# Performance work log

Measured on AMD Instinct MI355X. Metric: run time of the kernel, lower is better.

## Reference

```python
import jax, jax.numpy as jnp
import numpy as np

N_NODES = 100000
N_EDGES = 1600000
D_FEAT = 32


def setup_inputs() -> dict:
    key = jax.random.key(0)
    k1, k2, k3 = jax.random.split(key, 3)
    return {
        "x_real": jax.random.normal(k1, (N_NODES, D_FEAT), dtype=jnp.float32),
        "x_imag": jax.random.normal(k2, (N_NODES, D_FEAT), dtype=jnp.float32),
        "edge_index": jax.random.randint(k3, (2, N_EDGES), 0, N_NODES, dtype=jnp.int64),
        "evolution_time": jnp.asarray(0.5, dtype=jnp.float32),
        "diffusion_strength": jnp.asarray(1.0, dtype=jnp.float32),
    }


def reference(x_real, x_imag, edge_index, evolution_time, diffusion_strength):
    eps = 1e-8
    num_nodes = x_real.shape[0]
    x = x_real + 1j * x_imag  # [N, D] complex64

    # add self loops
    loops = jnp.arange(num_nodes, dtype=edge_index.dtype)
    row = jnp.concatenate([edge_index[0], loops])  # [E+N]
    col = jnp.concatenate([edge_index[1], loops])  # [E+N]

    # symmetric degree normalization: deg computed over col (as in source)
    deg = jnp.zeros((num_nodes,), jnp.float32).at[col].add(1.0)
    deg_inv_sqrt = jnp.where(deg > 0, deg ** -0.5, 0.0)
    norm = (deg_inv_sqrt[row] * deg_inv_sqrt[col])[:, None]  # [E+N, 1]

    def propagate(h):
        # gather by col, scale, scatter-add by row
        msgs = h[col] * norm.astype(h.dtype)
        return jnp.zeros_like(h).at[row].add(msgs)

    first_order = propagate(x)
    coeff1 = 1j * (evolution_time * diffusion_strength)
    evolved = x + coeff1 * first_order

    # evolution_order >= 2 (second-order Taylor term)
    second_order = propagate(first_order)
    evolved = evolved + (coeff1 * coeff1) * 0.5 * second_order

    # per-node |psi|^2 weights, normalized to sum to num_nodes
    w = (evolved * jnp.conj(evolved)).real.sum(axis=-1, keepdims=True)  # [N,1]
    s = w.sum()
    w = jnp.where(s > eps, w / s * num_nodes, jnp.ones_like(w))
    return w, evolved
```

## Files before the change

### kernel.cpp

```cpp
#include <hip/hip_runtime.h>
#include <cstdint>
#include <cstddef>


#define TPB 256
#define BSL 64
#define CRANGE 16384
#define SRANGE 8192

typedef _Float16 h2 __attribute__((ext_vector_type(2)));

#if defined(__has_builtin)
#if __has_builtin(__builtin_amdgcn_fdot2)
#define HAS_FDOT2 1
#endif
#endif

__device__ __forceinline__ h2 u2h(uint32_t u) {
    union { uint32_t u; h2 h; } x; x.u = u; return x.h;
}
__device__ __forceinline__ uint32_t h2u(h2 h) {
    union { uint32_t u; h2 h; } x; x.h = h; return x.u;
}
__device__ __forceinline__ uint32_t packh(float re, float im) {
    h2 h; h.x = (_Float16)re; h.y = (_Float16)im; return h2u(h);
}
__device__ __forceinline__ void acc2(uint32_t p, float& aR, float& aI) {
#ifdef HAS_FDOT2
    h2 v = u2h(p);
    h2 LO; LO.x = (_Float16)1.0f; LO.y = (_Float16)0.0f;
    h2 HI; HI.x = (_Float16)0.0f; HI.y = (_Float16)1.0f;
    aR = __builtin_amdgcn_fdot2(v, LO, aR, false);
    aI = __builtin_amdgcn_fdot2(v, HI, aI, false);
#else
    h2 v = u2h(p);
    aR += (float)v.x;
    aI += (float)v.y;
#endif
}
__device__ __forceinline__ void acc4(uint4 p, float (&aR)[4], float (&aI)[4]) {
    acc2(p.x, aR[0], aI[0]);
    acc2(p.y, aR[1], aI[1]);
    acc2(p.z, aR[2], aI[2]);
    acc2(p.w, aR[3], aI[3]);
}

__device__ __forceinline__ int slice_len(int E) {
    return (((E + BSL - 1) / BSL) + 3) & ~3;
}

__global__ void k_cnt2(const int* __restrict__ col, const int* __restrict__ row,
                       int E, int Nw, uint32_t* __restrict__ parts_col,
                       uint32_t* __restrict__ parts_row) {
    __shared__ uint32_t sh[CRANGE / 2];
    int which = blockIdx.x & 1;
    int rb = blockIdx.x >> 1;
    int r = rb / BSL, b = rb % BSL;
    const int* keys = which ? row : col;
    uint32_t*  parts = which ? parts_row : parts_col;
    int rbase = r * CRANGE;
    for (int i = threadIdx.x; i < CRANGE / 2; i += TPB) sh[i] = 0;
    __syncthreads();
    int SL = slice_len(E);
    int s0 = b * SL, s1 = min(E, s0 + SL);
    int n = s1 - s0;
    if (n > 0) {
        const int4* k4 = (const int4*)(keys + s0);
        int n4 = n >> 2;
        for (int j = threadIdx.x; j < n4; j += TPB) {
            int4 v = k4[j];
            int k;
            k = v.x - rbase; if ((unsigned)k < CRANGE) atomicAdd(&sh[k >> 1], 1u << ((k & 1) * 16));
            k = v.y - rbase; if ((unsigned)k < CRANGE) atomicAdd(&sh[k >> 1], 1u << ((k & 1) * 16));
            k = v.z - rbase; if ((unsigned)k < CRANGE) atomicAdd(&sh[k >> 1], 1u << ((k & 1) * 16));
            k = v.w - rbase; if ((unsigned)k < CRANGE) atomicAdd(&sh[k >> 1], 1u << ((k & 1) * 16));
        }
        for (int e = s0 + (n4 << 2) + threadIdx.x; e < s1; e += TPB) {
            int k = keys[e] - rbase;
            if ((unsigned)k < CRANGE) atomicAdd(&sh[k >> 1], 1u << ((k & 1) * 16));
        }
    }
    __syncthreads();
    int wbase = rbase >> 1;
    for (int i = threadIdx.x; i < CRANGE / 2; i += TPB) {
        int w = wbase + i;
        if (w < Nw) parts[(size_t)b * Nw + w] = sh[i];
    }
}

__global__ void k_discol(const uint32_t* __restrict__ parts, int Nw, int N,
                         float* __restrict__ dis) {
    int w = blockIdx.x * blockDim.x + threadIdx.x;
    if (w >= Nw) return;
    uint32_t lo = 0, hi = 0;
    for (int b = 0; b < BSL; ++b) {
        uint32_t v = parts[(size_t)b * Nw + w];
        lo += v & 0xFFFFu; hi += v >> 16;
    }
    int n = 2 * w;
    if (n < N)     dis[n]     = rsqrtf((float)lo + 1.0f);
    if (n + 1 < N) dis[n + 1] = rsqrtf((float)hi + 1.0f);
}

__global__ void k_redrow(const uint32_t* __restrict__ parts, int Nw, int N,
                         unsigned char* __restrict__ sliceoff,
                         int* __restrict__ rowcnt) {
    int w = blockIdx.x * blockDim.x + threadIdx.x;
    if (w >= Nw) return;
    uint32_t lo = 0, hi = 0;
    int n = 2 * w;
    for (int b = 0; b < BSL; ++b) {
        uint32_t v = parts[(size_t)b * Nw + w];
        if (n < N)     sliceoff[(size_t)b * N + n]     = (unsigned char)lo;
        if (n + 1 < N) sliceoff[(size_t)b * N + n + 1] = (unsigned char)hi;
        lo += v & 0xFFFFu; hi += v >> 16;
    }
    if (n < N)     rowcnt[n]     = (int)lo;
    if (n + 1 < N) rowcnt[n + 1] = (int)hi;
}

__global__ void k_scan1(const int* __restrict__ in, int* __restrict__ out,
                        int* __restrict__ partials, int N) {
    __shared__ int sh[256];
    int t = threadIdx.x;
    int base = blockIdx.x * 1024 + t * 4;
    int v0 = (base + 0 < N) ? in[base + 0] : 0;
    int v1 = (base + 1 < N) ? in[base + 1] : 0;
    int v2 = (base + 2 < N) ? in[base + 2] : 0;
    int v3 = (base + 3 < N) ? in[base + 3] : 0;
    int s = v0 + v1 + v2 + v3;
    sh[t] = s;
    __syncthreads();
    for (int off = 1; off < 256; off <<= 1) {
        int add = (t >= off) ? sh[t - off] : 0;
        __syncthreads();
        sh[t] += add;
        __syncthreads();
    }
    int excl = sh[t] - s;
    if (base + 0 < N) out[base + 0] = excl;
    excl += v0;
    if (base + 1 < N) out[base + 1] = excl;
    excl += v1;
    if (base + 2 < N) out[base + 2] = excl;
    excl += v2;
    if (base + 3 < N) out[base + 3] = excl;
    if (t == 255) partials[blockIdx.x] = sh[255];
}

__global__ void k_scan2(int* __restrict__ partials, int nb) {
    if (threadIdx.x == 0 && blockIdx.x == 0) {
        int acc = 0;
        for (int i = 0; i < nb; ++i) { int v = partials[i]; partials[i] = acc; acc += v; }
    }
}

__global__ void k_scan3(int* __restrict__ out, const int* __restrict__ partials,
                        int N, int E) {
    int i = blockIdx.x * blockDim.x + threadIdx.x;
    if (i < N) out[i] += partials[i >> 10];
    if (i == 0) out[N] = E;
}

__global__ void k_scatter2(const int* __restrict__ row, const int* __restrict__ col,
                           int E, int N, const int* __restrict__ rowptr,
                           const unsigned char* __restrict__ sliceoff,
                           int* __restrict__ ecol) {
    __shared__ int cur[SRANGE];
    int r = blockIdx.x / BSL, b = blockIdx.x % BSL;
    int rbase = r * SRANGE;
    for (int i = threadIdx.x; i < SRANGE; i += TPB) {
        int n = rbase + i;
        cur[i] = (n < N) ? rowptr[n] + (int)sliceoff[(size_t)b * N + n] : 0;
    }
    __syncthreads();
    int SL = slice_len(E);
    int s0 = b * SL, s1 = min(E, s0 + SL);
    int n = s1 - s0;
    if (n <= 0) return;
    const int4* r4 = (const int4*)(row + s0);
    const int4* c4 = (const int4*)(col + s0);
    int n4 = n >> 2;
    for (int j = threadIdx.x; j < n4; j += TPB) {
        int4 rv = r4[j];
        int4 cv = c4[j];
        int rr;
        rr = rv.x - rbase; if ((unsigned)rr < SRANGE) ecol[atomicAdd(&cur[rr], 1)] = cv.x;
        rr = rv.y - rbase; if ((unsigned)rr < SRANGE) ecol[atomicAdd(&cur[rr], 1)] = cv.y;
        rr = rv.z - rbase; if ((unsigned)rr < SRANGE) ecol[atomicAdd(&cur[rr], 1)] = cv.z;
        rr = rv.w - rbase; if ((unsigned)rr < SRANGE) ecol[atomicAdd(&cur[rr], 1)] = cv.w;
    }
    for (int e = s0 + (n4 << 2) + threadIdx.x; e < s1; e += TPB) {
        int rr = row[e] - rbase;
        if ((unsigned)rr < SRANGE) ecol[atomicAdd(&cur[rr], 1)] = col[e];
    }
}

__global__ void k_pack(const float* __restrict__ xr, const float* __restrict__ xi,
                       const float* __restrict__ dis, uint32_t* __restrict__ xds,
                       int N) {
    int i = blockIdx.x * blockDim.x + threadIdx.x;
    if (i < N * 32) {
        int n = i >> 5, k = i & 31, s = k >> 3, dd = k & 7;
        float dg = dis[n];
        xds[((size_t)s * N + n) * 8 + dd] = packh(xr[i] * dg, xi[i] * dg);
    }
}

__device__ __forceinline__ void edge_accum4(const int* __restrict__ ecol,
                                            const uint4* __restrict__ hb4,
                                            int beg, int end, int epos, int half,
                                            float (&aR)[4], float (&aI)[4]) {
    int base = beg;
    for (; base + 16 <= end; base += 16) {
        int c0 = ecol[base + epos];
        int c1 = ecol[base + epos + 4];
        int c2 = ecol[base + epos + 8];
        int c3 = ecol[base + epos + 12];
        uint4 p0 = hb4[(size_t)c0 * 2 + half];
        uint4 p1 = hb4[(size_t)c1 * 2 + half];
        uint4 p2 = hb4[(size_t)c2 * 2 + half];
        uint4 p3 = hb4[(size_t)c3 * 2 + half];
        acc4(p0, aR, aI); acc4(p1, aR, aI);
        acc4(p2, aR, aI); acc4(p3, aR, aI);
    }
    if (base + 8 <= end) {
        int c0 = ecol[base + epos];
        int c1 = ecol[base + epos + 4];
        uint4 p0 = hb4[(size_t)c0 * 2 + half];
        uint4 p1 = hb4[(size_t)c1 * 2 + half];
        acc4(p0, aR, aI); acc4(p1, aR, aI);
        base += 8;
    }
    int rem = end - base;
    if (epos < rem) {
        int c = ecol[base + epos];
        uint4 p = hb4[(size_t)c * 2 + half];
        acc4(p, aR, aI);
    }
    if (epos + 4 < rem) {
        int c = ecol[base + epos + 4];
        uint4 p = hb4[(size_t)c * 2 + half];
        acc4(p, aR, aI);
    }
}

__device__ __forceinline__ void reduce8(float (&aR)[4], float (&aI)[4]) {
    #pragma unroll
    for (int d = 0; d < 4; ++d) {
        aR[d] += __shfl_xor(aR[d], 2, 8);
        aI[d] += __shfl_xor(aI[d], 2, 8);
        aR[d] += __shfl_xor(aR[d], 4, 8);
        aI[d] += __shfl_xor(aI[d], 4, 8);
    }
}

__global__ void k_p1(const int* __restrict__ rowptr, const int* __restrict__ ecol,
                     const float* __restrict__ dis, const uint32_t* __restrict__ xds,
                     uint32_t* __restrict__ fo2b, uint32_t* __restrict__ fods, int N) {
    int s   = blockIdx.x & 3;
    int nb  = blockIdx.x >> 2;
    int r   = nb * 32 + (threadIdx.x >> 3);
    int sub = threadIdx.x & 7;
    int half = sub & 1, epos = sub >> 1;
    if (r >= N) return;
    const uint4* hb4 = (const uint4*)(xds + (size_t)s * N * 8);
    int beg = rowptr[r], end = rowptr[r + 1];
    float dg = dis[r];
    float aR[4] = {0.f, 0.f, 0.f, 0.f}, aI[4] = {0.f, 0.f, 0.f, 0.f};
    edge_accum4(ecol, hb4, beg, end, epos, half, aR, aI);
    reduce8(aR, aI);
    acc4(hb4[(size_t)r * 2 + half], aR, aI);
    if (epos == 0) {
        float foR[4], foI[4];
        #pragma unroll
        for (int d = 0; d < 4; ++d) { foR[d] = dg * aR[d]; foI[d] = dg * aI[d]; }
        uint4 f, fd;
        f.x = packh(foR[0], foI[0]); f.y = packh(foR[1], foI[1]);
        f.z = packh(foR[2], foI[2]); f.w = packh(foR[3], foI[3]);
        fd.x = packh(foR[0] * dg, foI[0] * dg); fd.y = packh(foR[1] * dg, foI[1] * dg);
        fd.z = packh(foR[2] * dg, foI[2] * dg); fd.w = packh(foR[3] * dg, foI[3] * dg);
        ((uint4*)(fo2b + (size_t)s * N * 8))[(size_t)r * 2 + half] = f;
        ((uint4*)(fods + (size_t)s * N * 8))[(size_t)r * 2 + half] = fd;
    }
}

__global__ void k_p2(const int* __restrict__ rowptr, const int* __restrict__ ecol,
                     const float* __restrict__ dis, const uint32_t* __restrict__ fo2b,
                     const uint32_t* __restrict__ fods,
                     const float* __restrict__ tptr, const float* __restrict__ dptr,
                     uint32_t* __restrict__ delta, int N) {
    int s   = blockIdx.x & 3;
    int nb  = blockIdx.x >> 2;
    int r   = nb * 32 + (threadIdx.x >> 3);
    int sub = threadIdx.x & 7;
    int half = sub & 1, epos = sub >> 1;
    if (r >= N) return;
    const uint4* hb4 = (const uint4*)(fods + (size_t)s * N * 8);
    int beg = rowptr[r], end = rowptr[r + 1];
    float dg = dis[r];
    float aR[4] = {0.f, 0.f, 0.f, 0.f}, aI[4] = {0.f, 0.f, 0.f, 0.f};
    edge_accum4(ecol, hb4, beg, end, epos, half, aR, aI);
    reduce8(aR, aI);
    acc4(hb4[(size_t)r * 2 + half], aR, aI);
    if (epos == 0) {
        float c1  = tptr[0] * dptr[0];
        float c2h = 0.5f * c1 * c1;
        uint4 f = ((const uint4*)(fo2b + (size_t)s * N * 8))[(size_t)r * 2 + half];
        uint32_t fv[4] = {f.x, f.y, f.z, f.w};
        uint4 dlt;
        uint32_t dv[4];
        #pragma unroll
        for (int d = 0; d < 4; ++d) {
            float soR = dg * aR[d], soI = dg * aI[d];
            h2 fo = u2h(fv[d]);
            float foR = (float)fo.x, foI = (float)fo.y;
            dv[d] = packh(-c1 * foI - c2h * soR, c1 * foR - c2h * soI);
        }
        dlt.x = dv[0]; dlt.y = dv[1]; dlt.z = dv[2]; dlt.w = dv[3];
        ((uint4*)(delta + (size_t)s * N * 8))[(size_t)r * 2 + half] = dlt;
    }
}

__global__ void k_final(const float* __restrict__ xr, const float* __restrict__ xi,
                        const uint32_t* __restrict__ delta, float* __restrict__ out,
                        int N, int interleaved, float* __restrict__ partials2) {
    int t = blockIdx.x * blockDim.x + threadIdx.x;
    int n = t >> 2, s = t & 3;
    float wsum = 0.f;
    if (n < N) {
        const uint4* dp = (const uint4*)(delta + ((size_t)s * N + n) * 8);
        uint4 d0 = dp[0], d1 = dp[1];
        size_t ib = (size_t)n * 32 + (size_t)s * 8;
        const float4* xr4 = (const float4*)(xr + ib);
        const float4* xi4 = (const float4*)(xi + ib);
        float4 a0 = xr4[0], a1 = xr4[1];
        float4 b0 = xi4[0], b1 = xi4[1];
        uint32_t dv[8] = {d0.x, d0.y, d0.z, d0.w, d1.x, d1.y, d1.z, d1.w};
        float ar[8] = {a0.x, a0.y, a0.z, a0.w, a1.x, a1.y, a1.z, a1.w};
        float ai[8] = {b0.x, b0.y, b0.z, b0.w, b1.x, b1.y, b1.z, b1.w};
        float er[8], ei[8];
        #pragma unroll
        for (int k = 0; k < 8; ++k) {
            h2 d = u2h(dv[k]);
            er[k] = ar[k] + (float)d.x;
            ei[k] = ai[k] + (float)d.y;
            wsum += er[k] * er[k] + ei[k] * ei[k];
        }
        if (interleaved) {
            float4* op = (float4*)(out + N + 2 * ib);
            op[0] = make_float4(er[0], ei[0], er[1], ei[1]);
            op[1] = make_float4(er[2], ei[2], er[3], ei[3]);
            op[2] = make_float4(er[4], ei[4], er[5], ei[5]);
            op[3] = make_float4(er[6], ei[6], er[7], ei[7]);
        } else {
            float4* op = (float4*)(out + N + ib);
            op[0] = make_float4(er[0], er[1], er[2], er[3]);
            op[1] = make_float4(er[4], er[5], er[6], er[7]);
        }
    }
    float nodesum = wsum;
    nodesum += __shfl_xor(nodesum, 1, 4);
    nodesum += __shfl_xor(nodesum, 2, 4);
    if (n < N && s == 0) out[n] = nodesum;
    float bv = wsum;
    #pragma unroll
    for (int off = 32; off; off >>= 1) bv += __shfl_xor(bv, off, 64);
    __shared__ float ls[TPB / 64];
    if ((threadIdx.x & 63) == 0) ls[threadIdx.x >> 6] = bv;
    __syncthreads();
    if (threadIdx.x == 0) {
        float bs = 0.f;
        #pragma unroll
        for (int i = 0; i < TPB / 64; ++i) bs += ls[i];
        partials2[blockIdx.x] = bs;
    }
}

__global__ void k_sum(const float* __restrict__ partials2, int nb,
                      float* __restrict__ S) {
    float acc = 0.f;
    for (int i = threadIdx.x; i < nb; i += blockDim.x) acc += partials2[i];
    #pragma unroll
    for (int off = 32; off; off >>= 1) acc += __shfl_xor(acc, off, 64);
    __shared__ float ls[TPB / 64];
    if ((threadIdx.x & 63) == 0) ls[threadIdx.x >> 6] = acc;
    __syncthreads();
    if (threadIdx.x == 0) {
        float s = 0.f;
        #pragma unroll
        for (int i = 0; i < TPB / 64; ++i) s += ls[i];
        *S = s;
    }
}

__global__ void k_norm(float* __restrict__ w, int N, const float* __restrict__ S) {
    int i = blockIdx.x * blockDim.x + threadIdx.x;
    if (i >= N) return;
    float s = *S;
    w[i] = (s > 1e-8f) ? w[i] * ((float)N / s) : 1.0f;
}

extern "C" void kernel_launch(void* const* d_in, const int* in_sizes, int n_in,
                              void* d_out, int out_size, void* d_ws, size_t ws_size,
                              hipStream_t stream) {
    const float* xr   = (const float*)d_in[0];
    const float* xi   = (const float*)d_in[1];
    const int*   eidx = (const int*)d_in[2];
    const float* tptr = (const float*)d_in[3];
    const float* dptr = (const float*)d_in[4];

    const int N = in_sizes[0] / 32;
    const int E = in_sizes[2] / 2;
    const int* row = eidx;
    const int* col = eidx + E;
    const long long ND = (long long)N * 32;
    const int Nw  = (N + 1) / 2;
    const int NB  = (N + 1023) / 1024;
    const int NBK = (N + 31) / 32;
    const int NFB = (int)((ND / 8 + TPB - 1) / TPB);
    const int NCR = (N + CRANGE - 1) / CRANGE;
    const int NSR = (N + SRANGE - 1) / SRANGE;

    size_t o = 0;
    auto alloc = [&](size_t words) {
        o = (o + 3) & ~(size_t)3;
        size_t r = o; o += words; return r;
    };
    uint32_t* wsw = (uint32_t*)d_ws;
    uint32_t*      parts_row = wsw + alloc((size_t)BSL * Nw);
    uint32_t*      parts_col = wsw + alloc((size_t)BSL * Nw);
    unsigned char* sliceoff  = (unsigned char*)(wsw + alloc(((size_t)BSL * N + 3) / 4));
    int*           rowcnt    = (int*)(wsw + alloc(N));
    int*           rowptr    = (int*)(wsw + alloc(N + 1));
    int*           partials  = (int*)(wsw + alloc(NB));
    float*         dis       = (float*)(wsw + alloc(N));
    uint32_t*      xds       = wsw + alloc(ND);
    uint32_t*      fo2b      = wsw + alloc(ND);
    uint32_t*      fods      = wsw + alloc(ND);
    float*         partials2 = (float*)(wsw + alloc(NFB));
    float*         S         = (float*)(wsw + alloc(1));
    uint32_t*      delta     = parts_row;
    int*           ecol      = (int*)parts_col;

    int interleaved = (out_size >= (int)(N + 2 * ND)) ? 1 : 0;
    float* out = (float*)d_out;

    k_cnt2<<<NCR * BSL * 2, TPB, 0, stream>>>(col, row, E, Nw, parts_col, parts_row);
    k_discol<<<(Nw + TPB - 1) / TPB, TPB, 0, stream>>>(parts_col, Nw, N, dis);
    k_redrow<<<(Nw + TPB - 1) / TPB, TPB, 0, stream>>>(parts_row, Nw, N,
                                                       sliceoff, rowcnt);
    k_scan1<<<NB, TPB, 0, stream>>>(rowcnt, rowptr, partials, N);
    k_scan2<<<1, 64, 0, stream>>>(partials, NB);
    k_scan3<<<(N + TPB - 1) / TPB, TPB, 0, stream>>>(rowptr, partials, N, E);
    k_scatter2<<<NSR * BSL, TPB, 0, stream>>>(row, col, E, N, rowptr,
                                              sliceoff, ecol);

    k_pack<<<(int)((ND + TPB - 1) / TPB), TPB, 0, stream>>>(xr, xi, dis, xds, N);
    int pgrid = 4 * NBK;
    k_p1<<<pgrid, TPB, 0, stream>>>(rowptr, ecol, dis, xds, fo2b, fods, N);
    k_p2<<<pgrid, TPB, 0, stream>>>(rowptr, ecol, dis, fo2b, fods, tptr, dptr,
                                    delta, N);
    k_final<<<NFB, TPB, 0, stream>>>(xr, xi, delta, out, N, interleaved, partials2);
    k_sum<<<1, TPB, 0, stream>>>(partials2, NFB, S);
    k_norm<<<(N + TPB - 1) / TPB, TPB, 0, stream>>>(out, N, S);
}
```

Baseline: 211.4 us.

## Pad CSR rows to multiples of 16 with a zero dummy node to drop tail handling

Row counts are rounded up to multiples of 16 in the scan, and ecol is prefilled with a dummy index N whose packed feature row is zero. The SpMM gather loop can then run full 16-edge steps with no remainder branches, and edge index loads become nontemporal. The cost is an extra fill pass over a larger ecol array (up to E+15N entries) and wasted gathers on padding, about 7.5 extra slots per row on average. The feature buffers grow by one node.

New measurement: 258.5 us. +22.3%, slower.

```diff
diff --git a/kernel.cpp b/kernel.cpp
--- a/kernel.cpp
+++ b/kernel.cpp
@@ -124,10 +124,10 @@
     __shared__ int sh[256];
     int t = threadIdx.x;
     int base = blockIdx.x * 1024 + t * 4;
-    int v0 = (base + 0 < N) ? in[base + 0] : 0;
-    int v1 = (base + 1 < N) ? in[base + 1] : 0;
-    int v2 = (base + 2 < N) ? in[base + 2] : 0;
-    int v3 = (base + 3 < N) ? in[base + 3] : 0;
+    int v0 = (base + 0 < N) ? ((in[base + 0] + 15) & ~15) : 0;
+    int v1 = (base + 1 < N) ? ((in[base + 1] + 15) & ~15) : 0;
+    int v2 = (base + 2 < N) ? ((in[base + 2] + 15) & ~15) : 0;
+    int v3 = (base + 3 < N) ? ((in[base + 3] + 15) & ~15) : 0;
     int s = v0 + v1 + v2 + v3;
     sh[t] = s;
     __syncthreads();
@@ -152,14 +152,20 @@
     if (threadIdx.x == 0 && blockIdx.x == 0) {
         int acc = 0;
         for (int i = 0; i < nb; ++i) { int v = partials[i]; partials[i] = acc; acc += v; }
+        partials[nb] = acc;
     }
 }
 
 __global__ void k_scan3(int* __restrict__ out, const int* __restrict__ partials,
-                        int N, int E) {
+                        int N, int nb) {
     int i = blockIdx.x * blockDim.x + threadIdx.x;
     if (i < N) out[i] += partials[i >> 10];
-    if (i == 0) out[N] = E;
+    if (i == 0) out[N] = partials[nb];
+}
+
+__global__ void k_fillN(int* __restrict__ ecol, long long total, int N) {
+    long long i = (long long)blockIdx.x * blockDim.x + threadIdx.x;
+    if (i < total) ecol[i] = N;
 }
 
 __global__ void k_scatter2(const int* __restrict__ row, const int* __restrict__ col,
@@ -198,50 +204,32 @@
 
 __global__ void k_pack(const float* __restrict__ xr, const float* __restrict__ xi,
                        const float* __restrict__ dis, uint32_t* __restrict__ xds,
-                       int N) {
+                       uint32_t* __restrict__ fods, int N) {
     int i = blockIdx.x * blockDim.x + threadIdx.x;
-    if (i < N * 32) {
-        int n = i >> 5, k = i & 31, s = k >> 3, dd = k & 7;
-        float dg = dis[n];
-        xds[((size_t)s * N + n) * 8 + dd] = packh(xr[i] * dg, xi[i] * dg);
-    }
+    int NP = N + 1;
+    if (i >= NP * 32) return;
+    int n = i >> 5, k = i & 31, s = k >> 3, dd = k & 7;
+    size_t o = ((size_t)s * NP + n) * 8 + dd;
+    if (n == N) { xds[o] = 0u; fods[o] = 0u; return; }
+    float dg = dis[n];
+    xds[o] = packh(xr[i] * dg, xi[i] * dg);
 }
 
 __device__ __forceinline__ void edge_accum4(const int* __restrict__ ecol,
                                             const uint4* __restrict__ hb4,
                                             int beg, int end, int epos, int half,
                                             float (&aR)[4], float (&aI)[4]) {
-    int base = beg;
-    for (; base + 16 <= end; base += 16) {
-        int c0 = ecol[base + epos];
-        int c1 = ecol[base + epos + 4];
-        int c2 = ecol[base + epos + 8];
-        int c3 = ecol[base + epos + 12];
+    for (int base = beg; base < end; base += 16) {
+        int c0 = __builtin_nontemporal_load(ecol + base + epos);
+        int c1 = __builtin_nontemporal_load(ecol + base + epos + 4);
+        int c2 = __builtin_nontemporal_load(ecol + base + epos + 8);
+        int c3 = __builtin_nontemporal_load(ecol + base + epos + 12);
         uint4 p0 = hb4[(size_t)c0 * 2 + half];
         uint4 p1 = hb4[(size_t)c1 * 2 + half];
         uint4 p2 = hb4[(size_t)c2 * 2 + half];
         uint4 p3 = hb4[(size_t)c3 * 2 + half];
         acc4(p0, aR, aI); acc4(p1, aR, aI);
         acc4(p2, aR, aI); acc4(p3, aR, aI);
-    }
-    if (base + 8 <= end) {
-        int c0 = ecol[base + epos];
-        int c1 = ecol[base + epos + 4];
-        uint4 p0 = hb4[(size_t)c0 * 2 + half];
-        uint4 p1 = hb4[(size_t)c1 * 2 + half];
-        acc4(p0, aR, aI); acc4(p1, aR, aI);
-        base += 8;
-    }
-    int rem = end - base;
-    if (epos < rem) {
-        int c = ecol[base + epos];
-        uint4 p = hb4[(size_t)c * 2 + half];
-        acc4(p, aR, aI);
-    }
-    if (epos + 4 < rem) {
-        int c = ecol[base + epos + 4];
-        uint4 p = hb4[(size_t)c * 2 + half];
-        acc4(p, aR, aI);
     }
 }
 
@@ -264,7 +252,8 @@
     int sub = threadIdx.x & 7;
     int half = sub & 1, epos = sub >> 1;
     if (r >= N) return;
-    const uint4* hb4 = (const uint4*)(xds + (size_t)s * N * 8);
+    size_t NP = (size_t)N + 1;
+    const uint4* hb4 = (const uint4*)(xds + (size_t)s * NP * 8);
     int beg = rowptr[r], end = rowptr[r + 1];
     float dg = dis[r];
     float aR[4] = {0.f, 0.f, 0.f, 0.f}, aI[4] = {0.f, 0.f, 0.f, 0.f};
@@ -280,8 +269,8 @@
         f.z = packh(foR[2], foI[2]); f.w = packh(foR[3], foI[3]);
         fd.x = packh(foR[0] * dg, foI[0] * dg); fd.y = packh(foR[1] * dg, foI[1] * dg);
         fd.z = packh(foR[2] * dg, foI[2] * dg); fd.w = packh(foR[3] * dg, foI[3] * dg);
-        ((uint4*)(fo2b + (size_t)s * N * 8))[(size_t)r * 2 + half] = f;
-        ((uint4*)(fods + (size_t)s * N * 8))[(size_t)r * 2 + half] = fd;
+        ((uint4*)(fo2b + (size_t)s * NP * 8))[(size_t)r * 2 + half] = f;
+        ((uint4*)(fods + (size_t)s * NP * 8))[(size_t)r * 2 + half] = fd;
     }
 }
 
@@ -296,7 +285,8 @@
     int sub = threadIdx.x & 7;
     int half = sub & 1, epos = sub >> 1;
     if (r >= N) return;
-    const uint4* hb4 = (const uint4*)(fods + (size_t)s * N * 8);
+    size_t NP = (size_t)N + 1;
+    const uint4* hb4 = (const uint4*)(fods + (size_t)s * NP * 8);
     int beg = rowptr[r], end = rowptr[r + 1];
     float dg = dis[r];
     float aR[4] = {0.f, 0.f, 0.f, 0.f}, aI[4] = {0.f, 0.f, 0.f, 0.f};
@@ -306,7 +296,12 @@
     if (epos == 0) {
         float c1  = tptr[0] * dptr[0];
         float c2h = 0.5f * c1 * c1;
-        uint4 f = ((const uint4*)(fo2b + (size_t)s * N * 8))[(size_t)r * 2 + half];
+        const uint4* fp = (const uint4*)(fo2b + (size_t)s * NP * 8);
+        uint4 f;
+        f.x = __builtin_nontemporal_load(&fp[(size_t)r * 2 + half].x);
+        f.y = __builtin_nontemporal_load(&fp[(size_t)r * 2 + half].y);
+        f.z = __builtin_nontemporal_load(&fp[(size_t)r * 2 + half].z);
+        f.w = __builtin_nontemporal_load(&fp[(size_t)r * 2 + half].w);
         uint32_t fv[4] = {f.x, f.y, f.z, f.w};
         uint4 dlt;
         uint32_t dv[4];
@@ -318,7 +313,7 @@
             dv[d] = packh(-c1 * foI - c2h * soR, c1 * foR - c2h * soI);
         }
         dlt.x = dv[0]; dlt.y = dv[1]; dlt.z = dv[2]; dlt.w = dv[3];
-        ((uint4*)(delta + (size_t)s * N * 8))[(size_t)r * 2 + half] = dlt;
+        ((uint4*)(delta + (size_t)s * NP * 8))[(size_t)r * 2 + half] = dlt;
     }
 }
 
@@ -327,9 +322,10 @@
                         int N, int interleaved, float* __restrict__ partials2) {
     int t = blockIdx.x * blockDim.x + threadIdx.x;
     int n = t >> 2, s = t & 3;
+    size_t NP = (size_t)N + 1;
     float wsum = 0.f;
     if (n < N) {
-        const uint4* dp = (const uint4*)(delta + ((size_t)s * N + n) * 8);
+        const uint4* dp = (const uint4*)(delta + ((size_t)s * NP + n) * 8);
         uint4 d0 = dp[0], d1 = dp[1];
         size_t ib = (size_t)n * 32 + (size_t)s * 8;
         const float4* xr4 = (const float4*)(xr + ib);
@@ -414,7 +410,9 @@
     const int E = in_sizes[2] / 2;
     const int* row = eidx;
     const int* col = eidx + E;
-    const long long ND = (long long)N * 32;
+    const long long ND  = (long long)N * 32;
+    const long long NDP = (long long)(N + 1) * 32;
+    const long long EPAD = (long long)E + 15LL * N;
     const int Nw  = (N + 1) / 2;
     const int NB  = (N + 1023) / 1024;
     const int NBK = (N + 31) / 32;
@@ -427,17 +425,21 @@
         o = (o + 3) & ~(size_t)3;
         size_t r = o; o += words; return r;
     };
+    size_t big_row = (size_t)BSL * Nw;
+    if (big_row < (size_t)NDP) big_row = (size_t)NDP;
+    size_t big_col = (size_t)BSL * Nw;
+    if (big_col < (size_t)EPAD) big_col = (size_t)EPAD;
     uint32_t* wsw = (uint32_t*)d_ws;
-    uint32_t*      parts_row = wsw + alloc((size_t)BSL * Nw);
-    uint32_t*      parts_col = wsw + alloc((size_t)BSL * Nw);
+    uint32_t*      parts_row = wsw + alloc(big_row);
+    uint32_t*      parts_col = wsw + alloc(big_col);
     unsigned char* sliceoff  = (unsigned char*)(wsw + alloc(((size_t)BSL * N + 3) / 4));
     int*           rowcnt    = (int*)(wsw + alloc(N));
     int*           rowptr    = (int*)(wsw + alloc(N + 1));
-    int*           partials  = (int*)(wsw + alloc(NB));
+    int*           partials  = (int*)(wsw + alloc(NB + 2));
     float*         dis       = (float*)(wsw + alloc(N));
-    uint32_t*      xds       = wsw + alloc(ND);
-    uint32_t*      fo2b      = wsw + alloc(ND);
-    uint32_t*      fods      = wsw + alloc(ND);
+    uint32_t*      xds       = wsw + alloc(NDP);
+    uint32_t*      fo2b      = wsw + alloc(NDP);
+    uint32_t*      fods      = wsw + alloc(NDP);
     float*         partials2 = (float*)(wsw + alloc(NFB));
     float*         S         = (float*)(wsw + alloc(1));
     uint32_t*      delta     = parts_row;
@@ -452,11 +454,13 @@
                                                        sliceoff, rowcnt);
     k_scan1<<<NB, TPB, 0, stream>>>(rowcnt, rowptr, partials, N);
     k_scan2<<<1, 64, 0, stream>>>(partials, NB);
-    k_scan3<<<(N + TPB - 1) / TPB, TPB, 0, stream>>>(rowptr, partials, N, E);
+    k_scan3<<<(N + TPB - 1) / TPB, TPB, 0, stream>>>(rowptr, partials, N, NB);
+    k_fillN<<<(int)((EPAD + TPB - 1) / TPB), TPB, 0, stream>>>(ecol, EPAD, N);
     k_scatter2<<<NSR * BSL, TPB, 0, stream>>>(row, col, E, N, rowptr,
                                               sliceoff, ecol);
 
-    k_pack<<<(int)((ND + TPB - 1) / TPB), TPB, 0, stream>>>(xr, xi, dis, xds, N);
+    k_pack<<<(int)((NDP + TPB - 1) / TPB), TPB, 0, stream>>>(xr, xi, dis, xds,
+                                                             fods, N);
     int pgrid = 4 * NBK;
     k_p1<<<pgrid, TPB, 0, stream>>>(rowptr, ecol, dis, xds, fo2b, fods, N);
     k_p2<<<pgrid, TPB, 0, stream>>>(rowptr, ecol, dis, fo2b, fods, tptr, dptr,
```

## Fuse final evolution into second propagation and pack scatter counters in shared memory

Applied to the files above, without the earlier changes.

The final combine step (x + delta, squared-norm weights, block partial sums) moves into the second propagation kernel. This removes the intermediate delta buffer and one launch, and first-order values are now recovered from fods by dividing by the degree factor instead of being stored in a separate fo2b buffer. The scatter kernel packs two 16-bit per-row counters into each shared word, which doubles the node range each block covers and halves the number of scatter blocks, at the cost of an extra rowptr gather per edge. Recovering first-order values from half-precision fods times 1/dg may lose some precision, and 16-bit counters assume fewer than 65536 entries per row per slice.

New measurement: 229.9 us. 1.09x slower.

```diff
diff --git a/kernel.cpp b/kernel.cpp
--- a/kernel.cpp
+++ b/kernel.cpp
@@ -6,7 +6,7 @@
 #define TPB 256
 #define BSL 64
 #define CRANGE 16384
-#define SRANGE 8192
+#define SRANGE 16384
 
 typedef _Float16 h2 __attribute__((ext_vector_type(2)));
 
@@ -166,12 +166,14 @@
                            int E, int N, const int* __restrict__ rowptr,
                            const unsigned char* __restrict__ sliceoff,
                            int* __restrict__ ecol) {
-    __shared__ int cur[SRANGE];
+    __shared__ uint32_t cur[SRANGE / 2];
     int r = blockIdx.x / BSL, b = blockIdx.x % BSL;
     int rbase = r * SRANGE;
-    for (int i = threadIdx.x; i < SRANGE; i += TPB) {
-        int n = rbase + i;
-        cur[i] = (n < N) ? rowptr[n] + (int)sliceoff[(size_t)b * N + n] : 0;
+    for (int i = threadIdx.x; i < SRANGE / 2; i += TPB) {
+        int n0 = rbase + 2 * i, n1 = n0 + 1;
+        uint32_t w0 = (n0 < N) ? (uint32_t)sliceoff[(size_t)b * N + n0] : 0u;
+        uint32_t w1 = (n1 < N) ? (uint32_t)sliceoff[(size_t)b * N + n1] : 0u;
+        cur[i] = w0 | (w1 << 16);
     }
     __syncthreads();
     int SL = slice_len(E);
@@ -184,15 +186,23 @@
     for (int j = threadIdx.x; j < n4; j += TPB) {
         int4 rv = r4[j];
         int4 cv = c4[j];
-        int rr;
-        rr = rv.x - rbase; if ((unsigned)rr < SRANGE) ecol[atomicAdd(&cur[rr], 1)] = cv.x;
-        rr = rv.y - rbase; if ((unsigned)rr < SRANGE) ecol[atomicAdd(&cur[rr], 1)] = cv.y;
-        rr = rv.z - rbase; if ((unsigned)rr < SRANGE) ecol[atomicAdd(&cur[rr], 1)] = cv.z;
-        rr = rv.w - rbase; if ((unsigned)rr < SRANGE) ecol[atomicAdd(&cur[rr], 1)] = cv.w;
+        #pragma unroll
+        for (int q = 0; q < 4; ++q) {
+            int rr = ((const int*)&rv)[q] - rbase;
+            if ((unsigned)rr < SRANGE) {
+                uint32_t old = atomicAdd(&cur[rr >> 1], 1u << ((rr & 1) * 16));
+                int off = (int)((old >> ((rr & 1) * 16)) & 0xFFFFu);
+                ecol[rowptr[rbase + rr] + off] = ((const int*)&cv)[q];
+            }
+        }
     }
     for (int e = s0 + (n4 << 2) + threadIdx.x; e < s1; e += TPB) {
         int rr = row[e] - rbase;
-        if ((unsigned)rr < SRANGE) ecol[atomicAdd(&cur[rr], 1)] = col[e];
+        if ((unsigned)rr < SRANGE) {
+            uint32_t old = atomicAdd(&cur[rr >> 1], 1u << ((rr & 1) * 16));
+            int off = (int)((old >> ((rr & 1) * 16)) & 0xFFFFu);
+            ecol[rowptr[rbase + rr] + off] = col[e];
+        }
     }
 }
 
@@ -257,7 +267,7 @@
 
 __global__ void k_p1(const int* __restrict__ rowptr, const int* __restrict__ ecol,
                      const float* __restrict__ dis, const uint32_t* __restrict__ xds,
-                     uint32_t* __restrict__ fo2b, uint32_t* __restrict__ fods, int N) {
+                     uint32_t* __restrict__ fods, int N) {
     int s   = blockIdx.x & 3;
     int nb  = blockIdx.x >> 2;
     int r   = nb * 32 + (threadIdx.x >> 3);
@@ -272,98 +282,70 @@
     reduce8(aR, aI);
     acc4(hb4[(size_t)r * 2 + half], aR, aI);
     if (epos == 0) {
-        float foR[4], foI[4];
-        #pragma unroll
-        for (int d = 0; d < 4; ++d) { foR[d] = dg * aR[d]; foI[d] = dg * aI[d]; }
-        uint4 f, fd;
-        f.x = packh(foR[0], foI[0]); f.y = packh(foR[1], foI[1]);
-        f.z = packh(foR[2], foI[2]); f.w = packh(foR[3], foI[3]);
-        fd.x = packh(foR[0] * dg, foI[0] * dg); fd.y = packh(foR[1] * dg, foI[1] * dg);
-        fd.z = packh(foR[2] * dg, foI[2] * dg); fd.w = packh(foR[3] * dg, foI[3] * dg);
-        ((uint4*)(fo2b + (size_t)s * N * 8))[(size_t)r * 2 + half] = f;
+        float dg2 = dg * dg;
+        uint4 fd;
+        fd.x = packh(dg2 * aR[0], dg2 * aI[0]);
+        fd.y = packh(dg2 * aR[1], dg2 * aI[1]);
+        fd.z = packh(dg2 * aR[2], dg2 * aI[2]);
+        fd.w = packh(dg2 * aR[3], dg2 * aI[3]);
         ((uint4*)(fods + (size_t)s * N * 8))[(size_t)r * 2 + half] = fd;
     }
 }
 
 __global__ void k_p2(const int* __restrict__ rowptr, const int* __restrict__ ecol,
-                     const float* __restrict__ dis, const uint32_t* __restrict__ fo2b,
-                     const uint32_t* __restrict__ fods,
+                     const float* __restrict__ dis, const uint32_t* __restrict__ fods,
+                     const float* __restrict__ xr, const float* __restrict__ xi,
                      const float* __restrict__ tptr, const float* __restrict__ dptr,
-                     uint32_t* __restrict__ delta, int N) {
+                     float* __restrict__ out, int N, int interleaved,
+                     float* __restrict__ ws4, float* __restrict__ partials2) {
     int s   = blockIdx.x & 3;
     int nb  = blockIdx.x >> 2;
     int r   = nb * 32 + (threadIdx.x >> 3);
     int sub = threadIdx.x & 7;
     int half = sub & 1, epos = sub >> 1;
-    if (r >= N) return;
-    const uint4* hb4 = (const uint4*)(fods + (size_t)s * N * 8);
-    int beg = rowptr[r], end = rowptr[r + 1];
-    float dg = dis[r];
-    float aR[4] = {0.f, 0.f, 0.f, 0.f}, aI[4] = {0.f, 0.f, 0.f, 0.f};
-    edge_accum4(ecol, hb4, beg, end, epos, half, aR, aI);
-    reduce8(aR, aI);
-    acc4(hb4[(size_t)r * 2 + half], aR, aI);
-    if (epos == 0) {
-        float c1  = tptr[0] * dptr[0];
-        float c2h = 0.5f * c1 * c1;
-        uint4 f = ((const uint4*)(fo2b + (size_t)s * N * 8))[(size_t)r * 2 + half];
-        uint32_t fv[4] = {f.x, f.y, f.z, f.w};
-        uint4 dlt;
-        uint32_t dv[4];
-        #pragma unroll
-        for (int d = 0; d < 4; ++d) {
-            float soR = dg * aR[d], soI = dg * aI[d];
-            h2 fo = u2h(fv[d]);
-            float foR = (float)fo.x, foI = (float)fo.y;
-            dv[d] = packh(-c1 * foI - c2h * soR, c1 * foR - c2h * soI);
+    bool valid = r < N;
+    float wc = 0.f;
+    if (valid) {
+        const uint4* hb4 = (const uint4*)(fods + (size_t)s * N * 8);
+        int beg = rowptr[r], end = rowptr[r + 1];
+        float dg = dis[r];
+        float aR[4] = {0.f, 0.f, 0.f, 0.f}, aI[4] = {0.f, 0.f, 0.f, 0.f};
+        edge_accum4(ecol, hb4, beg, end, epos, half, aR, aI);
+        reduce8(aR, aI);
+        uint4 fv4 = hb4[(size_t)r * 2 + half];
+        acc4(fv4, aR, aI);
+        if (epos == 0) {
+            float c1  = tptr[0] * dptr[0];
+            float c2h = 0.5f * c1 * c1;
+            float inv = 1.0f / dg;
+            size_t ib = (size_t)r * 32 + (size_t)s * 8 + (size_t)half * 4;
+            float4 a = *(const float4*)(xr + ib);
+            float4 bI = *(const float4*)(xi + ib);
+            float xrv[4] = {a.x, a.y, a.z, a.w};
+            float xiv[4] = {bI.x, bI.y, bI.z, bI.w};
+            uint32_t fu[4] = {fv4.x, fv4.y, fv4.z, fv4.w};
+            float er[4], ei[4];
+            #pragma unroll
+            for (int d = 0; d < 4; ++d) {
+                float soR = dg * aR[d], soI = dg * aI[d];
+                h2 f = u2h(fu[d]);
+                float foR = (float)f.x * inv, foI = (float)f.y * inv;
+                er[d] = xrv[d] - c1 * foI - c2h * soR;
+                ei[d] = xiv[d] + c1 * foR - c2h * soI;
+                wc += er[d] * er[d] + ei[d] * ei[d];
+            }
+            if (interleaved) {
+                float4* op = (float4*)(out + N + 2 * ib);
+                op[0] = make_float4(er[0], ei[0], er[1], ei[1]);
+                op[1] = make_float4(er[2], ei[2], er[3], ei[3]);
+            } else {
+                *(float4*)(out + N + ib) = make_float4(er[0], er[1], er[2], er[3]);
+            }
         }
-        dlt.x = dv[0]; dlt.y = dv[1]; dlt.z = dv[2]; dlt.w = dv[3];
-        ((uint4*)(delta + (size_t)s * N * 8))[(size_t)r * 2 + half] = dlt;
-    }
-}
-
-__global__ void k_final(const float* __restrict__ xr, const float* __restrict__ xi,
-                        const uint32_t* __restrict__ delta, float* __restrict__ out,
-                        int N, int interleaved, float* __restrict__ partials2) {
-    int t = blockIdx.x * blockDim.x + threadIdx.x;
-    int n = t >> 2, s = t & 3;
-    float wsum = 0.f;
-    if (n < N) {
-        const uint4* dp = (const uint4*)(delta + ((size_t)s * N + n) * 8);
-        uint4 d0 = dp[0], d1 = dp[1];
-        size_t ib = (size_t)n * 32 + (size_t)s * 8;
-        const float4* xr4 = (const float4*)(xr + ib);
-        const float4* xi4 = (const float4*)(xi + ib);
-        float4 a0 = xr4[0], a1 = xr4[1];
-        float4 b0 = xi4[0], b1 = xi4[1];
-        uint32_t dv[8] = {d0.x, d0.y, d0.z, d0.w, d1.x, d1.y, d1.z, d1.w};
-        float ar[8] = {a0.x, a0.y, a0.z, a0.w, a1.x, a1.y, a1.z, a1.w};
-        float ai[8] = {b0.x, b0.y, b0.z, b0.w, b1.x, b1.y, b1.z, b1.w};
-        float er[8], ei[8];
-        #pragma unroll
-        for (int k = 0; k < 8; ++k) {
-            h2 d = u2h(dv[k]);
-            er[k] = ar[k] + (float)d.x;
-            ei[k] = ai[k] + (float)d.y;
-            wsum += er[k] * er[k] + ei[k] * ei[k];
-        }
-        if (interleaved) {
-            float4* op = (float4*)(out + N + 2 * ib);
-            op[0] = make_float4(er[0], ei[0], er[1], ei[1]);
-            op[1] = make_float4(er[2], ei[2], er[3], ei[3]);
-            op[2] = make_float4(er[4], ei[4], er[5], ei[5]);
-            op[3] = make_float4(er[6], ei[6], er[7], ei[7]);
-        } else {
-            float4* op = (float4*)(out + N + ib);
-            op[0] = make_float4(er[0], er[1], er[2], er[3]);
-            op[1] = make_float4(er[4], er[5], er[6], er[7]);
-        }
-    }
-    float nodesum = wsum;
-    nodesum += __shfl_xor(nodesum, 1, 4);
-    nodesum += __shfl_xor(nodesum, 2, 4);
-    if (n < N && s == 0) out[n] = nodesum;
-    float bv = wsum;
+    }
+    float wpair = wc + __shfl_xor(wc, 1, 8);
+    if (valid && sub == 0) ws4[(size_t)s * N + r] = wpair;
+    float bv = wc;
     #pragma unroll
     for (int off = 32; off; off >>= 1) bv += __shfl_xor(bv, off, 64);
     __shared__ float ls[TPB / 64];
@@ -394,11 +376,14 @@
     }
 }
 
-__global__ void k_norm(float* __restrict__ w, int N, const float* __restrict__ S) {
+__global__ void k_wnorm(const float* __restrict__ ws4, float* __restrict__ out,
+                        int N, const float* __restrict__ S) {
     int i = blockIdx.x * blockDim.x + threadIdx.x;
     if (i >= N) return;
     float s = *S;
-    w[i] = (s > 1e-8f) ? w[i] * ((float)N / s) : 1.0f;
+    float wsum = ws4[i] + ws4[(size_t)N + i] + ws4[2 * (size_t)N + i] +
+                 ws4[3 * (size_t)N + i];
+    out[i] = (s > 1e-8f) ? wsum * ((float)N / s) : 1.0f;
 }
 
 extern "C" void kernel_launch(void* const* d_in, const int* in_sizes, int n_in,
@@ -418,9 +403,9 @@
     const int Nw  = (N + 1) / 2;
     const int NB  = (N + 1023) / 1024;
     const int NBK = (N + 31) / 32;
-    const int NFB = (int)((ND / 8 + TPB - 1) / TPB);
     const int NCR = (N + CRANGE - 1) / CRANGE;
     const int NSR = (N + SRANGE - 1) / SRANGE;
+    const int pgrid = 4 * NBK;
 
     size_t o = 0;
     auto alloc = [&](size_t words) {
@@ -433,14 +418,13 @@
     unsigned char* sliceoff  = (unsigned char*)(wsw + alloc(((size_t)BSL * N + 3) / 4));
     int*           rowcnt    = (int*)(wsw + alloc(N));
     int*           rowptr    = (int*)(wsw + alloc(N + 1));
-    int*           partials  = (int*)(wsw + alloc(NB));
+    int*           partials  = (int*)(wsw + alloc(NB + 2));
     float*         dis       = (float*)(wsw + alloc(N));
     uint32_t*      xds       = wsw + alloc(ND);
-    uint32_t*      fo2b      = wsw + alloc(ND);
     uint32_t*      fods      = wsw + alloc(ND);
-    float*         partials2 = (float*)(wsw + alloc(NFB));
+    float*         ws4       = (float*)(wsw + alloc((size_t)4 * N));
+    float*         partials2 = (float*)(wsw + alloc(pgrid));
     float*         S         = (float*)(wsw + alloc(1));
-    uint32_t*      delta     = parts_row;
     int*           ecol      = (int*)parts_col;
 
     int interleaved = (out_size >= (int)(N + 2 * ND)) ? 1 : 0;
@@ -457,11 +441,9 @@
                                               sliceoff, ecol);
 
     k_pack<<<(int)((ND + TPB - 1) / TPB), TPB, 0, stream>>>(xr, xi, dis, xds, N);
-    int pgrid = 4 * NBK;
-    k_p1<<<pgrid, TPB, 0, stream>>>(rowptr, ecol, dis, xds, fo2b, fods, N);
-    k_p2<<<pgrid, TPB, 0, stream>>>(rowptr, ecol, dis, fo2b, fods, tptr, dptr,
-                                    delta, N);
-    k_final<<<NFB, TPB, 0, stream>>>(xr, xi, delta, out, N, interleaved, partials2);
-    k_sum<<<1, TPB, 0, stream>>>(partials2, NFB, S);
-    k_norm<<<(N + TPB - 1) / TPB, TPB, 0, stream>>>(out, N, S);
-}
+    k_p1<<<pgrid, TPB, 0, stream>>>(rowptr, ecol, dis, xds, fods, N);
+    k_p2<<<pgrid, TPB, 0, stream>>>(rowptr, ecol, dis, fods, xr, xi, tptr, dptr,
+                                    out, N, interleaved, ws4, partials2);
+    k_sum<<<1, TPB, 0, stream>>>(partials2, pgrid, S);
+    k_wnorm<<<(N + TPB - 1) / TPB, TPB, 0, stream>>>(ws4, out, N, S);
+}
```

## Pack counters into 8-bit lanes, widen ranges, drop separate first-order buffer

Applied to the files above, without the earlier changes.

Counting histograms now pack four 8-bit counters per shared word, so each block covers a larger node range with twice as many edge slices. The scatter stage keeps packed per-slice offsets in LDS and adds rowptr at write time, which removes the byte sliceoff array and its per-node initialisation loads. The first propagation pass no longer writes a separate first-order buffer. The second pass recovers that value by dividing the dg²-scaled copy by dg, which saves one full-size write and read. The risks are 8-bit counter overflow if any row gets more than 255 edges in a slice, and extra fp16 rounding from the divide.

After: 196.1 us. 1.08x faster.

```diff
diff --git a/kernel.cpp b/kernel.cpp
--- a/kernel.cpp
+++ b/kernel.cpp
@@ -4,9 +4,9 @@
 
 
 #define TPB 256
-#define BSL 64
-#define CRANGE 16384
-#define SRANGE 8192
+#define BSL 128
+#define CRANGE 32768
+#define SRANGE 32768
 
 typedef _Float16 h2 __attribute__((ext_vector_type(2)));
 
@@ -50,16 +50,16 @@
 }
 
 __global__ void k_cnt2(const int* __restrict__ col, const int* __restrict__ row,
-                       int E, int Nw, uint32_t* __restrict__ parts_col,
+                       int E, int Nq, uint32_t* __restrict__ parts_col,
                        uint32_t* __restrict__ parts_row) {
-    __shared__ uint32_t sh[CRANGE / 2];
+    __shared__ uint32_t sh[CRANGE / 4];
     int which = blockIdx.x & 1;
     int rb = blockIdx.x >> 1;
     int r = rb / BSL, b = rb % BSL;
     const int* keys = which ? row : col;
     uint32_t*  parts = which ? parts_row : parts_col;
     int rbase = r * CRANGE;
-    for (int i = threadIdx.x; i < CRANGE / 2; i += TPB) sh[i] = 0;
+    for (int i = threadIdx.x; i < CRANGE / 4; i += TPB) sh[i] = 0;
     __syncthreads();
     int SL = slice_len(E);
     int s0 = b * SL, s1 = min(E, s0 + SL);
@@ -70,53 +70,58 @@
         for (int j = threadIdx.x; j < n4; j += TPB) {
             int4 v = k4[j];
             int k;
-            k = v.x - rbase; if ((unsigned)k < CRANGE) atomicAdd(&sh[k >> 1], 1u << ((k & 1) * 16));
-            k = v.y - rbase; if ((unsigned)k < CRANGE) atomicAdd(&sh[k >> 1], 1u << ((k & 1) * 16));
-            k = v.z - rbase; if ((unsigned)k < CRANGE) atomicAdd(&sh[k >> 1], 1u << ((k & 1) * 16));
-            k = v.w - rbase; if ((unsigned)k < CRANGE) atomicAdd(&sh[k >> 1], 1u << ((k & 1) * 16));
+            k = v.x - rbase; if ((unsigned)k < CRANGE) atomicAdd(&sh[k >> 2], 1u << ((k & 3) * 8));
+            k = v.y - rbase; if ((unsigned)k < CRANGE) atomicAdd(&sh[k >> 2], 1u << ((k & 3) * 8));
+            k = v.z - rbase; if ((unsigned)k < CRANGE) atomicAdd(&sh[k >> 2], 1u << ((k & 3) * 8));
+            k = v.w - rbase; if ((unsigned)k < CRANGE) atomicAdd(&sh[k >> 2], 1u << ((k & 3) * 8));
         }
         for (int e = s0 + (n4 << 2) + threadIdx.x; e < s1; e += TPB) {
             int k = keys[e] - rbase;
-            if ((unsigned)k < CRANGE) atomicAdd(&sh[k >> 1], 1u << ((k & 1) * 16));
-        }
-    }
-    __syncthreads();
-    int wbase = rbase >> 1;
-    for (int i = threadIdx.x; i < CRANGE / 2; i += TPB) {
+            if ((unsigned)k < CRANGE) atomicAdd(&sh[k >> 2], 1u << ((k & 3) * 8));
+        }
+    }
+    __syncthreads();
+    int wbase = rbase >> 2;
+    for (int i = threadIdx.x; i < CRANGE / 4; i += TPB) {
         int w = wbase + i;
-        if (w < Nw) parts[(size_t)b * Nw + w] = sh[i];
-    }
-}
-
-__global__ void k_discol(const uint32_t* __restrict__ parts, int Nw, int N,
+        if (w < Nq) parts[(size_t)b * Nq + w] = sh[i];
+    }
+}
+
+__global__ void k_discol(const uint32_t* __restrict__ parts, int Nq, int N,
                          float* __restrict__ dis) {
     int w = blockIdx.x * blockDim.x + threadIdx.x;
-    if (w >= Nw) return;
-    uint32_t lo = 0, hi = 0;
+    if (w >= Nq) return;
+    int c0 = 0, c1 = 0, c2 = 0, c3 = 0;
     for (int b = 0; b < BSL; ++b) {
-        uint32_t v = parts[(size_t)b * Nw + w];
-        lo += v & 0xFFFFu; hi += v >> 16;
-    }
-    int n = 2 * w;
-    if (n < N)     dis[n]     = rsqrtf((float)lo + 1.0f);
-    if (n + 1 < N) dis[n + 1] = rsqrtf((float)hi + 1.0f);
-}
-
-__global__ void k_redrow(const uint32_t* __restrict__ parts, int Nw, int N,
-                         unsigned char* __restrict__ sliceoff,
+        uint32_t v = parts[(size_t)b * Nq + w];
+        c0 += v & 255u; c1 += (v >> 8) & 255u; c2 += (v >> 16) & 255u; c3 += v >> 24;
+    }
+    int n = 4 * w;
+    if (n < N)     dis[n]     = rsqrtf((float)c0 + 1.0f);
+    if (n + 1 < N) dis[n + 1] = rsqrtf((float)c1 + 1.0f);
+    if (n + 2 < N) dis[n + 2] = rsqrtf((float)c2 + 1.0f);
+    if (n + 3 < N) dis[n + 3] = rsqrtf((float)c3 + 1.0f);
+}
+
+__global__ void k_redrow(const uint32_t* __restrict__ parts, int Nq, int N,
+                         uint32_t* __restrict__ sliceoff_w,
                          int* __restrict__ rowcnt) {
     int w = blockIdx.x * blockDim.x + threadIdx.x;
-    if (w >= Nw) return;
-    uint32_t lo = 0, hi = 0;
-    int n = 2 * w;
+    if (w >= Nq) return;
+    int c0 = 0, c1 = 0, c2 = 0, c3 = 0;
     for (int b = 0; b < BSL; ++b) {
-        uint32_t v = parts[(size_t)b * Nw + w];
-        if (n < N)     sliceoff[(size_t)b * N + n]     = (unsigned char)lo;
-        if (n + 1 < N) sliceoff[(size_t)b * N + n + 1] = (unsigned char)hi;
-        lo += v & 0xFFFFu; hi += v >> 16;
-    }
-    if (n < N)     rowcnt[n]     = (int)lo;
-    if (n + 1 < N) rowcnt[n + 1] = (int)hi;
+        uint32_t v = parts[(size_t)b * Nq + w];
+        sliceoff_w[(size_t)b * Nq + w] =
+            (uint32_t)c0 | ((uint32_t)c1 << 8) | ((uint32_t)c2 << 16) |
+            ((uint32_t)c3 << 24);
+        c0 += v & 255u; c1 += (v >> 8) & 255u; c2 += (v >> 16) & 255u; c3 += v >> 24;
+    }
+    int n = 4 * w;
+    if (n < N)     rowcnt[n]     = c0;
+    if (n + 1 < N) rowcnt[n + 1] = c1;
+    if (n + 2 < N) rowcnt[n + 2] = c2;
+    if (n + 3 < N) rowcnt[n + 3] = c3;
 }
 
 __global__ void k_scan1(const int* __restrict__ in, int* __restrict__ out,
@@ -163,16 +168,15 @@
 }
 
 __global__ void k_scatter2(const int* __restrict__ row, const int* __restrict__ col,
-                           int E, int N, const int* __restrict__ rowptr,
-                           const unsigned char* __restrict__ sliceoff,
+                           int E, int N, int Nq, const int* __restrict__ rowptr,
+                           const uint32_t* __restrict__ sliceoff_w,
                            int* __restrict__ ecol) {
-    __shared__ int cur[SRANGE];
+    __shared__ uint32_t cur[SRANGE / 4];
     int r = blockIdx.x / BSL, b = blockIdx.x % BSL;
     int rbase = r * SRANGE;
-    for (int i = threadIdx.x; i < SRANGE; i += TPB) {
-        int n = rbase + i;
-        cur[i] = (n < N) ? rowptr[n] + (int)sliceoff[(size_t)b * N + n] : 0;
-    }
+    int wb = rbase >> 2;
+    for (int i = threadIdx.x; i < SRANGE / 4; i += TPB)
+        cur[i] = (wb + i < Nq) ? sliceoff_w[(size_t)b * Nq + wb + i] : 0u;
     __syncthreads();
     int SL = slice_len(E);
     int s0 = b * SL, s1 = min(E, s0 + SL);
@@ -184,15 +188,23 @@
     for (int j = threadIdx.x; j < n4; j += TPB) {
         int4 rv = r4[j];
         int4 cv = c4[j];
-        int rr;
-        rr = rv.x - rbase; if ((unsigned)rr < SRANGE) ecol[atomicAdd(&cur[rr], 1)] = cv.x;
-        rr = rv.y - rbase; if ((unsigned)rr < SRANGE) ecol[atomicAdd(&cur[rr], 1)] = cv.y;
-        rr = rv.z - rbase; if ((unsigned)rr < SRANGE) ecol[atomicAdd(&cur[rr], 1)] = cv.z;
-        rr = rv.w - rbase; if ((unsigned)rr < SRANGE) ecol[atomicAdd(&cur[rr], 1)] = cv.w;
+        #pragma unroll
+        for (int q = 0; q < 4; ++q) {
+            int rr = ((const int*)&rv)[q] - rbase;
+            if ((unsigned)rr < SRANGE) {
+                uint32_t old = atomicAdd(&cur[rr >> 2], 1u << ((rr & 3) * 8));
+                int off = (int)((old >> ((rr & 3) * 8)) & 0xFFu);
+                ecol[rowptr[rbase + rr] + off] = ((const int*)&cv)[q];
+            }
+        }
     }
     for (int e = s0 + (n4 << 2) + threadIdx.x; e < s1; e += TPB) {
         int rr = row[e] - rbase;
-        if ((unsigned)rr < SRANGE) ecol[atomicAdd(&cur[rr], 1)] = col[e];
+        if ((unsigned)rr < SRANGE) {
+            uint32_t old = atomicAdd(&cur[rr >> 2], 1u << ((rr & 3) * 8));
+            int off = (int)((old >> ((rr & 3) * 8)) & 0xFFu);
+            ecol[rowptr[rbase + rr] + off] = col[e];
+        }
     }
 }
 
@@ -257,7 +269,7 @@
 
 __global__ void k_p1(const int* __restrict__ rowptr, const int* __restrict__ ecol,
                      const float* __restrict__ dis, const uint32_t* __restrict__ xds,
-                     uint32_t* __restrict__ fo2b, uint32_t* __restrict__ fods, int N) {
+                     uint32_t* __restrict__ fods, int N) {
     int s   = blockIdx.x & 3;
     int nb  = blockIdx.x >> 2;
     int r   = nb * 32 + (threadIdx.x >> 3);
@@ -272,22 +284,18 @@
     reduce8(aR, aI);
     acc4(hb4[(size_t)r * 2 + half], aR, aI);
     if (epos == 0) {
-        float foR[4], foI[4];
-        #pragma unroll
-        for (int d = 0; d < 4; ++d) { foR[d] = dg * aR[d]; foI[d] = dg * aI[d]; }
-        uint4 f, fd;
-        f.x = packh(foR[0], foI[0]); f.y = packh(foR[1], foI[1]);
-        f.z = packh(foR[2], foI[2]); f.w = packh(foR[3], foI[3]);
-        fd.x = packh(foR[0] * dg, foI[0] * dg); fd.y = packh(foR[1] * dg, foI[1] * dg);
-        fd.z = packh(foR[2] * dg, foI[2] * dg); fd.w = packh(foR[3] * dg, foI[3] * dg);
-        ((uint4*)(fo2b + (size_t)s * N * 8))[(size_t)r * 2 + half] = f;
+        float dg2 = dg * dg;
+        uint4 fd;
+        fd.x = packh(dg2 * aR[0], dg2 * aI[0]);
+        fd.y = packh(dg2 * aR[1], dg2 * aI[1]);
+        fd.z = packh(dg2 * aR[2], dg2 * aI[2]);
+        fd.w = packh(dg2 * aR[3], dg2 * aI[3]);
         ((uint4*)(fods + (size_t)s * N * 8))[(size_t)r * 2 + half] = fd;
     }
 }
 
 __global__ void k_p2(const int* __restrict__ rowptr, const int* __restrict__ ecol,
-                     const float* __restrict__ dis, const uint32_t* __restrict__ fo2b,
-                     const uint32_t* __restrict__ fods,
+                     const float* __restrict__ dis, const uint32_t* __restrict__ fods,
                      const float* __restrict__ tptr, const float* __restrict__ dptr,
                      uint32_t* __restrict__ delta, int N) {
     int s   = blockIdx.x & 3;
@@ -302,19 +310,20 @@
     float aR[4] = {0.f, 0.f, 0.f, 0.f}, aI[4] = {0.f, 0.f, 0.f, 0.f};
     edge_accum4(ecol, hb4, beg, end, epos, half, aR, aI);
     reduce8(aR, aI);
-    acc4(hb4[(size_t)r * 2 + half], aR, aI);
+    uint4 fv4 = hb4[(size_t)r * 2 + half];
+    acc4(fv4, aR, aI);
     if (epos == 0) {
         float c1  = tptr[0] * dptr[0];
         float c2h = 0.5f * c1 * c1;
-        uint4 f = ((const uint4*)(fo2b + (size_t)s * N * 8))[(size_t)r * 2 + half];
-        uint32_t fv[4] = {f.x, f.y, f.z, f.w};
+        float inv = 1.0f / dg;
+        uint32_t fu[4] = {fv4.x, fv4.y, fv4.z, fv4.w};
         uint4 dlt;
         uint32_t dv[4];
         #pragma unroll
         for (int d = 0; d < 4; ++d) {
             float soR = dg * aR[d], soI = dg * aI[d];
-            h2 fo = u2h(fv[d]);
-            float foR = (float)fo.x, foI = (float)fo.y;
+            h2 f = u2h(fu[d]);
+            float foR = (float)f.x * inv, foI = (float)f.y * inv;
             dv[d] = packh(-c1 * foI - c2h * soR, c1 * foR - c2h * soI);
         }
         dlt.x = dv[0]; dlt.y = dv[1]; dlt.z = dv[2]; dlt.w = dv[3];
@@ -415,52 +424,53 @@
     const int* row = eidx;
     const int* col = eidx + E;
     const long long ND = (long long)N * 32;
-    const int Nw  = (N + 1) / 2;
+    const int Nq  = (N + 3) / 4;
     const int NB  = (N + 1023) / 1024;
     const int NBK = (N + 31) / 32;
     const int NFB = (int)((ND / 8 + TPB - 1) / TPB);
     const int NCR = (N + CRANGE - 1) / CRANGE;
     const int NSR = (N + SRANGE - 1) / SRANGE;
+    const int pgrid = 4 * NBK;
 
     size_t o = 0;
     auto alloc = [&](size_t words) {
         o = (o + 3) & ~(size_t)3;
         size_t r = o; o += words; return r;
     };
+    size_t slab = (size_t)BSL * Nq;
+    size_t slab_row = slab < (size_t)ND ? (size_t)ND : slab;
+    size_t slab_col = slab < (size_t)E ? (size_t)E : slab;
     uint32_t* wsw = (uint32_t*)d_ws;
-    uint32_t*      parts_row = wsw + alloc((size_t)BSL * Nw);
-    uint32_t*      parts_col = wsw + alloc((size_t)BSL * Nw);
-    unsigned char* sliceoff  = (unsigned char*)(wsw + alloc(((size_t)BSL * N + 3) / 4));
-    int*           rowcnt    = (int*)(wsw + alloc(N));
-    int*           rowptr    = (int*)(wsw + alloc(N + 1));
-    int*           partials  = (int*)(wsw + alloc(NB));
-    float*         dis       = (float*)(wsw + alloc(N));
-    uint32_t*      xds       = wsw + alloc(ND);
-    uint32_t*      fo2b      = wsw + alloc(ND);
-    uint32_t*      fods      = wsw + alloc(ND);
-    float*         partials2 = (float*)(wsw + alloc(NFB));
-    float*         S         = (float*)(wsw + alloc(1));
-    uint32_t*      delta     = parts_row;
-    int*           ecol      = (int*)parts_col;
+    uint32_t* parts_row  = wsw + alloc(slab_row);
+    uint32_t* parts_col  = wsw + alloc(slab_col);
+    uint32_t* sliceoff_w = wsw + alloc(slab);
+    int*      rowcnt     = (int*)(wsw + alloc(N));
+    int*      rowptr     = (int*)(wsw + alloc(N + 1));
+    int*      partials   = (int*)(wsw + alloc(NB + 2));
+    float*    dis        = (float*)(wsw + alloc(N));
+    uint32_t* xds        = wsw + alloc(ND);
+    uint32_t* fods       = wsw + alloc(ND);
+    float*    partials2  = (float*)(wsw + alloc(NFB));
+    float*    S          = (float*)(wsw + alloc(1));
+    uint32_t* delta      = parts_row;
+    int*      ecol       = (int*)parts_col;
 
     int interleaved = (out_size >= (int)(N + 2 * ND)) ? 1 : 0;
     float* out = (float*)d_out;
 
-    k_cnt2<<<NCR * BSL * 2, TPB, 0, stream>>>(col, row, E, Nw, parts_col, parts_row);
-    k_discol<<<(Nw + TPB - 1) / TPB, TPB, 0, stream>>>(parts_col, Nw, N, dis);
-    k_redrow<<<(Nw + TPB - 1) / TPB, TPB, 0, stream>>>(parts_row, Nw, N,
-                                                       sliceoff, rowcnt);
+    k_cnt2<<<NCR * BSL * 2, TPB, 0, stream>>>(col, row, E, Nq, parts_col, parts_row);
+    k_discol<<<(Nq + TPB - 1) / TPB, TPB, 0, stream>>>(parts_col, Nq, N, dis);
+    k_redrow<<<(Nq + TPB - 1) / TPB, TPB, 0, stream>>>(parts_row, Nq, N,
+                                                       sliceoff_w, rowcnt);
     k_scan1<<<NB, TPB, 0, stream>>>(rowcnt, rowptr, partials, N);
     k_scan2<<<1, 64, 0, stream>>>(partials, NB);
     k_scan3<<<(N + TPB - 1) / TPB, TPB, 0, stream>>>(rowptr, partials, N, E);
-    k_scatter2<<<NSR * BSL, TPB, 0, stream>>>(row, col, E, N, rowptr,
-                                              sliceoff, ecol);
+    k_scatter2<<<NSR * BSL, TPB, 0, stream>>>(row, col, E, N, Nq, rowptr,
+                                              sliceoff_w, ecol);
 
     k_pack<<<(int)((ND + TPB - 1) / TPB), TPB, 0, stream>>>(xr, xi, dis, xds, N);
-    int pgrid = 4 * NBK;
-    k_p1<<<pgrid, TPB, 0, stream>>>(rowptr, ecol, dis, xds, fo2b, fods, N);
-    k_p2<<<pgrid, TPB, 0, stream>>>(rowptr, ecol, dis, fo2b, fods, tptr, dptr,
-                                    delta, N);
+    k_p1<<<pgrid, TPB, 0, stream>>>(rowptr, ecol, dis, xds, fods, N);
+    k_p2<<<pgrid, TPB, 0, stream>>>(rowptr, ecol, dis, fods, tptr, dptr, delta, N);
     k_final<<<NFB, TPB, 0, stream>>>(xr, xi, delta, out, N, interleaved, partials2);
     k_sum<<<1, TPB, 0, stream>>>(partials2, NFB, S);
     k_norm<<<(N + TPB - 1) / TPB, TPB, 0, stream>>>(out, N, S);
```
